# Performance work log

Measured on AMD Instinct MI355X. Metric: run time of the kernel, lower is better.

Reference implementation:

```python
import jax, jax.numpy as jnp
import numpy as np

COST_CLASS = 1.0
COST_BBOX = 5.0
COST_GIOU = 2.0


def box_cxcywh_to_xyxy(b):
    cx, cy, w, h = b[..., 0], b[..., 1], b[..., 2], b[..., 3]
    return jnp.stack([cx - 0.5 * w, cy - 0.5 * h, cx + 0.5 * w, cy + 0.5 * h], axis=-1)


def generalized_box_iou(boxes1, boxes2):
    # boxes1: [N,4] xyxy, boxes2: [M,4] xyxy -> [N,M]
    area1 = (boxes1[:, 2] - boxes1[:, 0]) * (boxes1[:, 3] - boxes1[:, 1])
    area2 = (boxes2[:, 2] - boxes2[:, 0]) * (boxes2[:, 3] - boxes2[:, 1])
    lt = jnp.maximum(boxes1[:, None, :2], boxes2[None, :, :2])  # [N,M,2]
    rb = jnp.minimum(boxes1[:, None, 2:], boxes2[None, :, 2:])
    wh = jnp.clip(rb - lt, 0.0)
    inter = wh[..., 0] * wh[..., 1]
    union = area1[:, None] + area2[None, :] - inter
    iou = inter / union
    lt_e = jnp.minimum(boxes1[:, None, :2], boxes2[None, :, :2])
    rb_e = jnp.maximum(boxes1[:, None, 2:], boxes2[None, :, 2:])
    wh_e = jnp.clip(rb_e - lt_e, 0.0)
    area_e = wh_e[..., 0] * wh_e[..., 1]
    return iou - (area_e - union) / area_e


def setup_inputs() -> dict:
    key = jax.random.key(0)
    k1, k2, k3, k4 = jax.random.split(key, 4)
    B, Q, C, T = 16, 900, 92, 1600
    pred_logits = jax.random.normal(k1, (B, Q, C), dtype=jnp.float32)
    pred_boxes = jax.random.uniform(k2, (B, Q, 4), dtype=jnp.float32)
    tgt_labels = jax.random.randint(k3, (T,), 0, C, dtype=jnp.int64)
    tgt_boxes = jax.random.uniform(k4, (T, 4), dtype=jnp.float32)
    return {"pred_logits": pred_logits, "pred_boxes": pred_boxes,
            "tgt_labels": tgt_labels, "tgt_boxes": tgt_boxes}


def reference(pred_logits, pred_boxes, tgt_labels, tgt_boxes):
    B, Q, C = pred_logits.shape
    out_prob = jax.nn.softmax(pred_logits.reshape(B * Q, C), axis=-1)  # [BQ,C]
    out_bbox = pred_boxes.reshape(B * Q, 4)
    # classification cost: -prob at the target class (gather over columns)
    cost_class = -out_prob[:, tgt_labels]  # [BQ,T]
    # L1 cdist between predicted and target boxes (cxcywh)
    cost_bbox = jnp.sum(jnp.abs(out_bbox[:, None, :] - tgt_bbox_expand(tgt_boxes)), axis=-1)
    # GIoU cost on xyxy boxes
    cost_giou = -generalized_box_iou(box_cxcywh_to_xyxy(out_bbox), box_cxcywh_to_xyxy(tgt_boxes))
    cost = COST_BBOX * cost_bbox + COST_CLASS * cost_class + COST_GIOU * cost_giou
    return cost.reshape(B, Q, -1)


def tgt_bbox_expand(tgt_boxes):
    return tgt_boxes[None, :, :]
```

## Files before the change

kernel.cpp:

```cpp
#include <hip/hip_runtime.h>
#include <hip/hip_bf16.h>
#include <math.h>


#define NTHR 320
#define RR   48
#define CC   92
#define CP   96

__global__ __launch_bounds__(NTHR) void detr_cost_kernel(
    const float* __restrict__ logits,
    const float* __restrict__ pboxes,
    const int*   __restrict__ labels,
    const float* __restrict__ tboxes,
    float*       __restrict__ out,
    int T)
{
    __shared__ float s_nprob[RR * CP];

    const int tid  = threadIdx.x;
    const int j    = blockIdx.x * NTHR + tid;
    const int row0 = blockIdx.y * RR;

    const float4 t = ((const float4*)tboxes)[j];
    const float tx1 = t.x - 0.5f * t.z;
    const float ty1 = t.y - 0.5f * t.w;
    const float tx2 = t.x + 0.5f * t.z;
    const float ty2 = t.y + 0.5f * t.w;
    const float ta  = t.z * t.w;
    const int   lbl = labels[j];

    const int wv = tid >> 6, ln = tid & 63;
    for (int rr = wv; rr < RR; rr += 5) {
        const float* lg = logits + (long long)(row0 + rr) * CC;
        float v1 = (ln < CC)      ? lg[ln]      : -INFINITY;
        float v2 = (ln + 64 < CC) ? lg[ln + 64] : -INFINITY;
        float m = fmaxf(v1, v2);
        #pragma unroll
        for (int o = 32; o > 0; o >>= 1) m = fmaxf(m, __shfl_xor(m, o));
        float e1 = (ln < CC)      ? __expf(v1 - m) : 0.0f;
        float e2 = (ln + 64 < CC) ? __expf(v2 - m) : 0.0f;
        float s = e1 + e2;
        #pragma unroll
        for (int o = 32; o > 0; o >>= 1) s += __shfl_xor(s, o);
        float inv = __builtin_amdgcn_rcpf(s);
        if (ln < CC)      s_nprob[rr * CP + ln]      = -e1 * inv;
        if (ln + 64 < CC) s_nprob[rr * CP + ln + 64] = -e2 * inv;
    }

    __syncthreads();

    const float4* pb4 = (const float4*)pboxes;
    #pragma unroll 4
    for (int r = 0; r < RR; ++r) {
        const float4 p = pb4[row0 + r];
        const float px1 = p.x - 0.5f * p.z;
        const float py1 = p.y - 0.5f * p.w;
        const float px2 = p.x + 0.5f * p.z;
        const float py2 = p.y + 0.5f * p.w;
        const float pa  = p.z * p.w;

        const float nprob = s_nprob[r * CP + lbl];

        const float l1 = fabsf(p.x - t.x) + fabsf(p.y - t.y)
                       + fabsf(p.z - t.z) + fabsf(p.w - t.w);

        const float iw    = fminf(px2, tx2) - fmaxf(px1, tx1);
        const float ih    = fminf(py2, ty2) - fmaxf(py1, ty1);
        const float inter = fmaxf(iw, 0.0f) * fmaxf(ih, 0.0f);
        const float uni   = pa + ta - inter;
        const float iou   = inter * __builtin_amdgcn_rcpf(uni);

        const float ew   = fmaxf(px2, tx2) - fminf(px1, tx1);
        const float eh   = fmaxf(py2, ty2) - fminf(py1, ty1);
        const float ea   = ew * eh;
        const float giou = iou - (ea - uni) * __builtin_amdgcn_rcpf(ea);

        out[(long long)(row0 + r) * T + j] = fmaf(5.0f, l1, nprob) - 2.0f * giou;
    }
}

extern "C" void kernel_launch(void* const* d_in, const int* in_sizes, int n_in,
                              void* d_out, int out_size, void* d_ws, size_t ws_size,
                              hipStream_t stream) {
    const float* logits = (const float*)d_in[0];
    const float* pboxes = (const float*)d_in[1];
    const int*   labels = (const int*)d_in[2];
    const float* tboxes = (const float*)d_in[3];
    float* out = (float*)d_out;

    const int T  = in_sizes[2];
    const int BQ = in_sizes[1] / 4;

    dim3 grid(T / NTHR, BQ / RR);
    detr_cost_kernel<<<grid, NTHR, 0, stream>>>(logits, pboxes, labels, tboxes, out, T);
}
```

Before: 137.1 us.

## Process four targets per thread with float4 stores and shared pred-box precompute

Each thread now handles four consecutive target columns, storing results as float4. Blocks shrink to 16 prediction rows. The grid has fewer column tiles, so each row's softmax is recomputed by fewer blocks. Predicted-box corners and areas are computed once per block into shared memory instead of per thread per row. The aim is wider memory transactions and less redundant softmax work. The cost is idle threads in the partial last column tile (T=1600 against a tile of 1024), and the code assumes T is a multiple of 4.

```diff
diff --git a/kernel.cpp b/kernel.cpp
--- a/kernel.cpp
+++ b/kernel.cpp
@@ -3,8 +3,10 @@
 #include <math.h>
 
 
-#define NTHR 320
-#define RR   48
+#define NTHR 256
+#define VEC  4
+#define TILE (NTHR * VEC)
+#define RR   16
 #define CC   92
 #define CP   96
 
@@ -16,22 +18,47 @@
     float*       __restrict__ out,
     int T)
 {
-    __shared__ float s_nprob[RR * CP];
+    __shared__ float  s_nprob[RR * CP];
+    __shared__ float4 s_pc[RR];
+    __shared__ float4 s_px[RR];
+    __shared__ float  s_pa[RR];
 
     const int tid  = threadIdx.x;
-    const int j    = blockIdx.x * NTHR + tid;
+    const int j0   = blockIdx.x * TILE + tid * VEC;
     const int row0 = blockIdx.y * RR;
+    const bool active = (j0 + VEC - 1) < T;
 
-    const float4 t = ((const float4*)tboxes)[j];
-    const float tx1 = t.x - 0.5f * t.z;
-    const float ty1 = t.y - 0.5f * t.w;
-    const float tx2 = t.x + 0.5f * t.z;
-    const float ty2 = t.y + 0.5f * t.w;
-    const float ta  = t.z * t.w;
-    const int   lbl = labels[j];
+    float tcx[VEC], tcy[VEC], tw[VEC], th[VEC];
+    float tx1[VEC], ty1[VEC], tx2[VEC], ty2[VEC], ta[VEC];
+    int   lbl[VEC];
+    if (active) {
+        const float4* tb4 = (const float4*)tboxes;
+        const int4 lb = *(const int4*)(labels + j0);
+        const int* lp = (const int*)&lb;
+        #pragma unroll
+        for (int u = 0; u < VEC; ++u) {
+            float4 t = tb4[j0 + u];
+            tcx[u] = t.x; tcy[u] = t.y; tw[u] = t.z; th[u] = t.w;
+            tx1[u] = t.x - 0.5f * t.z;
+            ty1[u] = t.y - 0.5f * t.w;
+            tx2[u] = t.x + 0.5f * t.z;
+            ty2[u] = t.y + 0.5f * t.w;
+            ta[u]  = t.z * t.w;
+            lbl[u] = lp[u];
+        }
+    }
+
+    if (tid < RR) {
+        float4 p = ((const float4*)pboxes)[row0 + tid];
+        float x1 = p.x - 0.5f * p.z, y1 = p.y - 0.5f * p.w;
+        float x2 = p.x + 0.5f * p.z, y2 = p.y + 0.5f * p.w;
+        s_pc[tid] = p;
+        s_px[tid] = make_float4(x1, y1, x2, y2);
+        s_pa[tid] = p.z * p.w;
+    }
 
     const int wv = tid >> 6, ln = tid & 63;
-    for (int rr = wv; rr < RR; rr += 5) {
+    for (int rr = wv; rr < RR; rr += 4) {
         const float* lg = logits + (long long)(row0 + rr) * CC;
         float v1 = (ln < CC)      ? lg[ln]      : -INFINITY;
         float v2 = (ln + 64 < CC) ? lg[ln + 64] : -INFINITY;
@@ -49,34 +76,37 @@
     }
 
     __syncthreads();
+    if (!active) return;
 
-    const float4* pb4 = (const float4*)pboxes;
-    #pragma unroll 4
+    float* outp = out + (long long)row0 * T + j0;
+    #pragma unroll 2
     for (int r = 0; r < RR; ++r) {
-        const float4 p = pb4[row0 + r];
-        const float px1 = p.x - 0.5f * p.z;
-        const float py1 = p.y - 0.5f * p.w;
-        const float px2 = p.x + 0.5f * p.z;
-        const float py2 = p.y + 0.5f * p.w;
-        const float pa  = p.z * p.w;
+        const float4 pc = s_pc[r];
+        const float4 px = s_px[r];
+        const float  pa = s_pa[r];
+        const float* np = &s_nprob[r * CP];
 
-        const float nprob = s_nprob[r * CP + lbl];
+        float4 res;
+        float* rp = (float*)&res;
+        #pragma unroll
+        for (int u = 0; u < VEC; ++u) {
+            const float l1 = fabsf(pc.x - tcx[u]) + fabsf(pc.y - tcy[u])
+                           + fabsf(pc.z - tw[u])  + fabsf(pc.w - th[u]);
 
-        const float l1 = fabsf(p.x - t.x) + fabsf(p.y - t.y)
-                       + fabsf(p.z - t.z) + fabsf(p.w - t.w);
+            const float iw    = fminf(px.z, tx2[u]) - fmaxf(px.x, tx1[u]);
+            const float ih    = fminf(px.w, ty2[u]) - fmaxf(px.y, ty1[u]);
+            const float inter = fmaxf(iw, 0.0f) * fmaxf(ih, 0.0f);
+            const float uni   = pa + ta[u] - inter;
+            const float iou   = inter * __builtin_amdgcn_rcpf(uni);
 
-        const float iw    = fminf(px2, tx2) - fmaxf(px1, tx1);
-        const float ih    = fminf(py2, ty2) - fmaxf(py1, ty1);
-        const float inter = fmaxf(iw, 0.0f) * fmaxf(ih, 0.0f);
-        const float uni   = pa + ta - inter;
-        const float iou   = inter * __builtin_amdgcn_rcpf(uni);
+            const float ew   = fmaxf(px.z, tx2[u]) - fminf(px.x, tx1[u]);
+            const float eh   = fmaxf(px.w, ty2[u]) - fminf(px.y, ty1[u]);
+            const float ea   = ew * eh;
+            const float giou = iou - (ea - uni) * __builtin_amdgcn_rcpf(ea);
 
-        const float ew   = fmaxf(px2, tx2) - fminf(px1, tx1);
-        const float eh   = fmaxf(py2, ty2) - fminf(py1, ty1);
-        const float ea   = ew * eh;
-        const float giou = iou - (ea - uni) * __builtin_amdgcn_rcpf(ea);
-
-        out[(long long)(row0 + r) * T + j] = fmaf(5.0f, l1, nprob) - 2.0f * giou;
+            rp[u] = fmaf(5.0f, l1, np[lbl[u]]) - 2.0f * giou;
+        }
+        *(float4*)(outp + (long long)r * T) = res;
     }
 }
 
@@ -92,6 +122,6 @@
     const int T  = in_sizes[2];
     const int BQ = in_sizes[1] / 4;
 
-    dim3 grid(T / NTHR, BQ / RR);
+    dim3 grid((T + TILE - 1) / TILE, BQ / RR);
     detr_cost_kernel<<<grid, NTHR, 0, stream>>>(logits, pboxes, labels, tboxes, out, T);
 }
```

Measured after the change: 126.4 us. -7.8%, faster.

## Split softmax into separate kernel and gather probabilities from workspace

Applied to the files above, without the earlier changes.

Splits the single fused kernel into two. A softmax kernel writes negated probabilities to a global workspace, and a cost kernel reads the per-label probability from that buffer (largely L2-resident) instead of from shared memory. This removes the softmax work that each block redid for its rows across all target tiles, and drops the shared-memory barrier. In exchange it adds a second launch, a global write and read of the probability matrix, and uncoalesced gathered loads in the cost kernel. The cost kernel also changes its tiling to 64 targets by 32 rows per 256-thread block, with the box loads hoisted into registers.

```diff
diff --git a/kernel.cpp b/kernel.cpp
--- a/kernel.cpp
+++ b/kernel.cpp
@@ -3,36 +3,20 @@
 #include <math.h>
 
 
-#define NTHR 320
-#define RR   48
-#define CC   92
-#define CP   96
+#define CC     92
+#define ROWS_A 16
+#define RW     8
+#define RR     32
 
-__global__ __launch_bounds__(NTHR) void detr_cost_kernel(
+__global__ __launch_bounds__(256) void softmax_kernel(
     const float* __restrict__ logits,
-    const float* __restrict__ pboxes,
-    const int*   __restrict__ labels,
-    const float* __restrict__ tboxes,
-    float*       __restrict__ out,
-    int T)
+    float*       __restrict__ nprob)
 {
-    __shared__ float s_nprob[RR * CP];
-
-    const int tid  = threadIdx.x;
-    const int j    = blockIdx.x * NTHR + tid;
-    const int row0 = blockIdx.y * RR;
-
-    const float4 t = ((const float4*)tboxes)[j];
-    const float tx1 = t.x - 0.5f * t.z;
-    const float ty1 = t.y - 0.5f * t.w;
-    const float tx2 = t.x + 0.5f * t.z;
-    const float ty2 = t.y + 0.5f * t.w;
-    const float ta  = t.z * t.w;
-    const int   lbl = labels[j];
-
-    const int wv = tid >> 6, ln = tid & 63;
-    for (int rr = wv; rr < RR; rr += 5) {
-        const float* lg = logits + (long long)(row0 + rr) * CC;
+    const int wv = threadIdx.x >> 6, ln = threadIdx.x & 63;
+    const int base = blockIdx.x * ROWS_A;
+    for (int rr = wv; rr < ROWS_A; rr += 4) {
+        const long long row = base + rr;
+        const float* lg = logits + row * CC;
         float v1 = (ln < CC)      ? lg[ln]      : -INFINITY;
         float v2 = (ln + 64 < CC) ? lg[ln + 64] : -INFINITY;
         float m = fmaxf(v1, v2);
@@ -44,23 +28,49 @@
         #pragma unroll
         for (int o = 32; o > 0; o >>= 1) s += __shfl_xor(s, o);
         float inv = __builtin_amdgcn_rcpf(s);
-        if (ln < CC)      s_nprob[rr * CP + ln]      = -e1 * inv;
-        if (ln + 64 < CC) s_nprob[rr * CP + ln + 64] = -e2 * inv;
+        if (ln < CC)      nprob[row * CC + ln]      = -e1 * inv;
+        if (ln + 64 < CC) nprob[row * CC + ln + 64] = -e2 * inv;
     }
+}
 
-    __syncthreads();
+__global__ __launch_bounds__(256) void cost_kernel(
+    const float* __restrict__ pboxes,
+    const int*   __restrict__ labels,
+    const float* __restrict__ tboxes,
+    const float* __restrict__ nprob,
+    float*       __restrict__ out,
+    int T)
+{
+    const int ln = threadIdx.x & 63;
+    const int wv = threadIdx.x >> 6;
+    const int j    = blockIdx.x * 64 + ln;
+    const int row0 = blockIdx.y * RR + wv * RW;
 
-    const float4* pb4 = (const float4*)pboxes;
-    #pragma unroll 4
-    for (int r = 0; r < RR; ++r) {
-        const float4 p = pb4[row0 + r];
+    const float4 t = ((const float4*)tboxes)[j];
+    const float tx1 = t.x - 0.5f * t.z;
+    const float ty1 = t.y - 0.5f * t.w;
+    const float tx2 = t.x + 0.5f * t.z;
+    const float ty2 = t.y + 0.5f * t.w;
+    const float ta  = t.z * t.w;
+    const int   lbl = labels[j];
+
+    const float* np = nprob + (long long)row0 * CC + lbl;
+    float*      op  = out   + (long long)row0 * T  + j;
+
+    float4 pc[RW];
+    #pragma unroll
+    for (int r = 0; r < RW; ++r) pc[r] = ((const float4*)pboxes)[row0 + r];
+
+    #pragma unroll
+    for (int r = 0; r < RW; ++r) {
+        const float4 p = pc[r];
         const float px1 = p.x - 0.5f * p.z;
         const float py1 = p.y - 0.5f * p.w;
         const float px2 = p.x + 0.5f * p.z;
         const float py2 = p.y + 0.5f * p.w;
         const float pa  = p.z * p.w;
 
-        const float nprob = s_nprob[r * CP + lbl];
+        const float nprb = np[r * CC];
 
         const float l1 = fabsf(p.x - t.x) + fabsf(p.y - t.y)
                        + fabsf(p.z - t.z) + fabsf(p.w - t.w);
@@ -76,7 +86,7 @@
         const float ea   = ew * eh;
         const float giou = iou - (ea - uni) * __builtin_amdgcn_rcpf(ea);
 
-        out[(long long)(row0 + r) * T + j] = fmaf(5.0f, l1, nprob) - 2.0f * giou;
+        op[r * T] = fmaf(5.0f, l1, nprb) - 2.0f * giou;
     }
 }
 
@@ -87,11 +97,14 @@
     const float* pboxes = (const float*)d_in[1];
     const int*   labels = (const int*)d_in[2];
     const float* tboxes = (const float*)d_in[3];
-    float* out = (float*)d_out;
+    float* out   = (float*)d_out;
+    float* nprob = (float*)d_ws;
 
     const int T  = in_sizes[2];
     const int BQ = in_sizes[1] / 4;
 
-    dim3 grid(T / NTHR, BQ / RR);
-    detr_cost_kernel<<<grid, NTHR, 0, stream>>>(logits, pboxes, labels, tboxes, out, T);
+    softmax_kernel<<<BQ / ROWS_A, 256, 0, stream>>>(logits, nprob);
+
+    dim3 grid(T / 64, BQ / RR);
+    cost_kernel<<<grid, 256, 0, stream>>>(pboxes, labels, tboxes, nprob, out, T);
 }
```

Result: faster. 130.8 us (-4.6%).
